# Performance work log

Hardware: AMD Instinct MI355X
Metric: run time of the kernel (lower is better)

## Reference

```python
import jax, jax.numpy as jnp
import numpy as np

B, N, M, C = 4, 4096, 300, 1152
SA_H, SA_D = 36, 32           # linear self-attention heads / head dim
CA_H = 16                     # cross-attention heads
INNER_SA = SA_H * SA_D        # 1152
INNER_FF = int(C * 2.5)       # 2880
EPS = 1e-6


def _ln(x):
    # LayerNorm without affine, eps=1e-6
    mu = x.mean(-1, keepdims=True)
    var = x.var(-1, keepdims=True)
    return (x - mu) / jnp.sqrt(var + EPS)


def setup_inputs() -> dict:
    key = jax.random.key(0)
    ks = jax.random.split(key, 24)
    p = lambda i, shape: jax.random.normal(ks[i], shape, jnp.float32) * 0.02
    return {
        "x": jax.random.normal(ks[0], (B, N, C), jnp.float32),
        "conditioning": jax.random.normal(ks[1], (B, M, C), jnp.float32),
        "t_emb": jax.random.normal(ks[2], (B, C), jnp.float32),
        # linear self-attention (qkv has no bias)
        "w_qkv": p(3, (C, 3 * INNER_SA)),
        "w_sa_out": p(4, (INNER_SA, C)),
        "b_sa_out": jnp.zeros((C,), jnp.float32),
        # norm_cross (affine LayerNorm)
        "gamma_cross": jnp.ones((C,), jnp.float32),
        "beta_cross": jnp.zeros((C,), jnp.float32),
        # cross-attention
        "w_q": p(5, (C, C)), "b_q": jnp.zeros((C,), jnp.float32),
        "w_kv": p(6, (C, 2 * C)), "b_kv": jnp.zeros((2 * C,), jnp.float32),
        "w_co": p(7, (C, C)), "b_co": jnp.zeros((C,), jnp.float32),
        # MixFFN
        "w_fc1": p(8, (C, 2 * INNER_FF)), "b_fc1": jnp.zeros((2 * INNER_FF,), jnp.float32),
        "dw_kernel": p(9, (3, 3, 1, INNER_FF)),  # depthwise conv, HWIO
        "dw_bias": jnp.zeros((INNER_FF,), jnp.float32),
        "w_fc2": p(10, (INNER_FF, C)), "b_fc2": jnp.zeros((C,), jnp.float32),
        # adaLN modulation
        "w_ada": p(11, (C, 6 * C)), "b_ada": jnp.zeros((6 * C,), jnp.float32),
        "sst": jax.random.normal(ks[12], (6, C), jnp.float32) * 0.02,
    }


def reference(x, conditioning, t_emb, w_qkv, w_sa_out, b_sa_out,
              gamma_cross, beta_cross, w_q, b_q, w_kv, b_kv, w_co, b_co,
              w_fc1, b_fc1, dw_kernel, dw_bias, w_fc2, b_fc2,
              w_ada, b_ada, sst):
    Bx, Nx, Cx = x.shape
    ada = jax.nn.silu(t_emb) @ w_ada + b_ada          # (B, 6C)
    ada = sst[None] + ada.reshape(Bx, 6, Cx)          # (B, 6, C)
    shift_sa, scale_sa, gate_sa, shift_ff, scale_ff, gate_ff = (
        ada[:, 0], ada[:, 1], ada[:, 2], ada[:, 3], ada[:, 4], ada[:, 5])

    # --- modulated linear self-attention (ReLU kernel) ---
    xn = _ln(x) * (1.0 + scale_sa[:, None]) + shift_sa[:, None]
    qkv = (xn @ w_qkv).reshape(Bx, Nx, 3, SA_H, SA_D)
    q = jax.nn.relu(qkv[:, :, 0])
    k = jax.nn.relu(qkv[:, :, 1])
    v = qkv[:, :, 2]
    kv = jnp.einsum('bnhd,bnhe->bhde', k, v)                  # (B,H,D,D)
    out = jnp.einsum('bnhd,bhde->bnhe', q, kv)                # (B,N,H,D)
    denom = jnp.einsum('bnhd,bhd->bnh', q, k.sum(1)) + 1e-6   # (B,N,H)
    out = (out / denom[..., None]).reshape(Bx, Nx, INNER_SA)
    x = x + gate_sa[:, None] * (out @ w_sa_out + b_sa_out)

    # --- cross-attention (softmax) ---
    xc = _ln(x) * gamma_cross + beta_cross
    hd = Cx // CA_H
    qc = (xc @ w_q + b_q).reshape(Bx, Nx, CA_H, hd)
    kvc = (conditioning @ w_kv + b_kv).reshape(Bx, M, 2, CA_H, hd)
    kc, vc = kvc[:, :, 0], kvc[:, :, 1]
    attn = jnp.einsum('bnhd,bmhd->bhnm', qc, kc) * (hd ** -0.5)
    attn = jax.nn.softmax(attn, axis=-1)
    oc = jnp.einsum('bhnm,bmhd->bnhd', attn, vc).reshape(Bx, Nx, Cx)
    x = x + oc @ w_co + b_co

    # --- modulated GLU-dwconv FFN ---
    xn = _ln(x) * (1.0 + scale_ff[:, None]) + shift_ff[:, None]
    gv = xn @ w_fc1 + b_fc1
    gate, val = gv[..., :INNER_FF], gv[..., INNER_FF:]
    h = jax.nn.silu(gate) * val
    hw = int(round(Nx ** 0.5))
    h = h.reshape(Bx, hw, hw, INNER_FF)                       # NHWC
    h = jax.lax.conv_general_dilated(
        h, dw_kernel, window_strides=(1, 1), padding='SAME',
        dimension_numbers=('NHWC', 'HWIO', 'NHWC'),
        feature_group_count=INNER_FF) + dw_bias
    h = h.reshape(Bx, Nx, INNER_FF)
    x = x + gate_ff[:, None] * (h @ w_fc2 + b_fc2)
    return x
```

## Files before the change

### kernel.cpp

```cpp
#include <hip/hip_runtime.h>

typedef __bf16 bf16_t;
typedef __attribute__((ext_vector_type(8))) __bf16 bf16x8;
typedef __attribute__((ext_vector_type(4))) __bf16 bf16x4;
typedef __attribute__((ext_vector_type(4))) float f32x4;

#define DEVINL __device__ __forceinline__

DEVINL void gload16(const void* g, void* l) {
  __builtin_amdgcn_global_load_lds(
      (const __attribute__((address_space(1))) void*)g,
      (__attribute__((address_space(3))) void*)l, 16, 0, 0);
}

template <int OUT>
__global__ __launch_bounds__(256) void gemm_bt(
    const bf16_t* __restrict__ A, const bf16_t* __restrict__ Bt,
    void* __restrict__ Cv, int M, int N, int K,
    long strideA, long strideB, long strideC,
    const float* __restrict__ bias, const float* __restrict__ resid,
    const float* __restrict__ gate, int GM)
{
  __shared__ __align__(16) bf16_t sA[128 * 32];
  __shared__ __align__(16) bf16_t sB[128 * 32];
  const int tid = threadIdx.x;
  const int lane = tid & 63;
  const int wave = tid >> 6;
  const bf16_t* Ab = A + (size_t)blockIdx.z * strideA;
  const bf16_t* Bb = Bt + (size_t)blockIdx.z * strideB;

  const int nbx = gridDim.x, nby = gridDim.y;
  const int nwg = nbx * nby;
  int lin = (int)blockIdx.y * nbx + (int)blockIdx.x;
  {
    const int q = nwg >> 3, r = nwg & 7;
    const int xcd = lin & 7, idx = lin >> 3;
    lin = (xcd < r ? xcd * (q + 1) : r * (q + 1) + (xcd - r) * q) + idx;
  }
  const int per_grp = GM * nbx;
  const int gid = lin / per_grp;
  const int rem = lin - gid * per_grp;
  const int gsz = min(GM, nby - gid * GM);
  const int byy = gid * GM + rem % gsz;
  const int bxx = rem / gsz;
  const long tileM = (long)byy * 128;
  const long tileN = (long)bxx * 128;
  const int wr = wave >> 1, wc = wave & 1;

  f32x4 acc[4][4] = {};

  const int srow = lane >> 2;
  const int skcol = (lane & 3) * 8;
  const bf16_t* gA0 = Ab + (tileM + wave * 16 + srow) * (long)K + skcol;
  const bf16_t* gB0 = Bb + (tileN + wave * 16 + srow) * (long)K + skcol;
  bf16_t* lA0 = sA + wave * 512;
  bf16_t* lB0 = sB + wave * 512;
  const long rs64 = 64L * K;

  const int aoff = (wr * 64 + (lane & 15)) * 32 + (lane >> 4) * 8;
  const int boff = (wc * 64 + (lane & 15)) * 32 + (lane >> 4) * 8;

  for (int kt = 0; kt < K; kt += 32) {
    __syncthreads();
    gload16(gA0 + kt, lA0);
    gload16(gA0 + kt + rs64, lA0 + 2048);
    gload16(gB0 + kt, lB0);
    gload16(gB0 + kt + rs64, lB0 + 2048);
    __syncthreads();
    bf16x8 av[4], bv[4];
#pragma unroll
    for (int m = 0; m < 4; ++m) av[m] = *(const bf16x8*)&sA[aoff + m * 512];
#pragma unroll
    for (int n = 0; n < 4; ++n) bv[n] = *(const bf16x8*)&sB[boff + n * 512];
#pragma unroll
    for (int m = 0; m < 4; ++m)
#pragma unroll
      for (int n = 0; n < 4; ++n)
        acc[m][n] = __builtin_amdgcn_mfma_f32_16x16x32_bf16(av[m], bv[n],
                                                            acc[m][n], 0, 0, 0);
  }

  const long row0 = tileM + wr * 64 + ((lane >> 4) * 4);
  const int col0 = (int)tileN + wc * 64 + (lane & 15);
#pragma unroll
  for (int m = 0; m < 4; ++m) {
#pragma unroll
    for (int n = 0; n < 4; ++n) {
      const int col = col0 + n * 16;
      const float bb = (OUT != 2 && bias) ? bias[col] : 0.0f;
#pragma unroll
      for (int j = 0; j < 4; ++j) {
        const long row = row0 + m * 16 + j;
        const float v = acc[m][n][j] + bb;
        if constexpr (OUT == 1) {
          const long idx = row * (long)N + col;
          const float g = gate ? gate[(row >> 12) * 6912 + col] : 1.0f;
          const float r = resid ? resid[idx] : 0.0f;
          ((float*)Cv)[idx] = r + g * v;
        } else if constexpr (OUT == 2) {
          if (col < 72)
            ((bf16_t*)Cv)[row * 1152 + (long)blockIdx.z * 72 + col] = (bf16_t)v;
        } else {
          const long idx = row * (long)N + col;
          (((bf16_t*)Cv) + (size_t)blockIdx.z * strideC)[idx] = (bf16_t)v;
        }
      }
    }
  }
}

__global__ __launch_bounds__(256) void transpose_cast(
    const float* __restrict__ W, bf16_t* __restrict__ WT, int K, int N)
{
  __shared__ float tile[32][33];
  const int n0 = blockIdx.x * 32, k0 = blockIdx.y * 32;
  const int tx = threadIdx.x & 31, ty = threadIdx.x >> 5;
#pragma unroll
  for (int r = ty; r < 32; r += 8) tile[r][tx] = W[(size_t)(k0 + r) * N + n0 + tx];
  __syncthreads();
#pragma unroll
  for (int r = ty; r < 32; r += 8)
    WT[(size_t)(n0 + r) * K + k0 + tx] = (bf16_t)tile[tx][r];
}

__global__ __launch_bounds__(256) void ada_kernel(
    const float* __restrict__ t_emb, const float* __restrict__ w_ada,
    const float* __restrict__ b_ada, const float* __restrict__ sst,
    float* __restrict__ ada)
{
  __shared__ float st[4][1152];
  const int t = threadIdx.x;
  const int j = blockIdx.x * 256 + t;
  for (int i = t; i < 4 * 1152; i += 256) {
    const int b = i / 1152, cc = i % 1152;
    const float v = t_emb[b * 1152 + cc];
    st[b][cc] = v / (1.0f + __expf(-v));
  }
  __syncthreads();
  const int k0 = blockIdx.y * 144;
  float a0 = 0.f, a1 = 0.f, a2 = 0.f, a3 = 0.f;
  for (int k = k0; k < k0 + 144; ++k) {
    const float w = w_ada[(size_t)k * 6912 + j];
    a0 += st[0][k] * w; a1 += st[1][k] * w;
    a2 += st[2][k] * w; a3 += st[3][k] * w;
  }
  if (blockIdx.y == 0) {
    const float base = b_ada[j] + sst[j];
    a0 += base; a1 += base; a2 += base; a3 += base;
  }
  atomicAdd(&ada[0 * 6912 + j], a0);
  atomicAdd(&ada[1 * 6912 + j], a1);
  atomicAdd(&ada[2 * 6912 + j], a2);
  atomicAdd(&ada[3 * 6912 + j], a3);
}

__global__ __launch_bounds__(256) void ln_mod(
    const float* __restrict__ X, bf16_t* __restrict__ out,
    const float* __restrict__ adaB, int shiftIdx, int scaleIdx,
    const float* __restrict__ gamma, const float* __restrict__ beta)
{
  const int row = blockIdx.x;
  const float4* xr4 = (const float4*)(X + (size_t)row * 1152);
  float s = 0.f, s2 = 0.f;
  for (int i = threadIdx.x; i < 288; i += 256) {
    const float4 v = xr4[i];
    s += v.x + v.y + v.z + v.w;
    s2 += v.x * v.x + v.y * v.y + v.z * v.z + v.w * v.w;
  }
  const int lane = threadIdx.x & 63, wave = threadIdx.x >> 6;
#pragma unroll
  for (int o = 32; o; o >>= 1) { s += __shfl_down(s, o); s2 += __shfl_down(s2, o); }
  __shared__ float rs[4], rq[4];
  if (lane == 0) { rs[wave] = s; rq[wave] = s2; }
  __syncthreads();
  if (threadIdx.x == 0) {
    rs[0] = rs[0] + rs[1] + rs[2] + rs[3];
    rq[0] = rq[0] + rq[1] + rq[2] + rq[3];
  }
  __syncthreads();
  const float mu = rs[0] * (1.0f / 1152.0f);
  const float var = rq[0] * (1.0f / 1152.0f) - mu * mu;
  const float inv = rsqrtf(var + 1e-6f);
  const int b = row >> 12;
  const float4* shiftv = (const float4*)(adaB ? adaB + b * 6912 + shiftIdx * 1152 : beta);
  const float4* scalev = (const float4*)(adaB ? adaB + b * 6912 + scaleIdx * 1152 : gamma);
  const float add1 = adaB ? 1.0f : 0.0f;
  for (int i = threadIdx.x; i < 288; i += 256) {
    const float4 v = xr4[i];
    const float4 sc = scalev[i];
    const float4 sh = shiftv[i];
    bf16x4 o;
    o[0] = (bf16_t)((v.x - mu) * inv * (add1 + sc.x) + sh.x);
    o[1] = (bf16_t)((v.y - mu) * inv * (add1 + sc.y) + sh.y);
    o[2] = (bf16_t)((v.z - mu) * inv * (add1 + sc.z) + sh.z);
    o[3] = (bf16_t)((v.w - mu) * inv * (add1 + sc.w) + sh.w);
    *(bf16x4*)&out[(size_t)row * 1152 + i * 4] = o;
  }
}

__global__ void pad_cond_k(const float* __restrict__ cond, bf16_t* __restrict__ condp)
{
  const int idx = blockIdx.x * 256 + threadIdx.x;
  const int row = idx / 1152;
  condp[idx] = (row < 1200) ? (bf16_t)cond[idx] : (bf16_t)0.0f;
}

__global__ __launch_bounds__(256) void sa_kv_k(
    const bf16_t* __restrict__ qkv, float* __restrict__ kvb, float* __restrict__ ksumb)
{
  const int bh = blockIdx.x, b = bh / 36, h = bh % 36;
  __shared__ bf16_t sk[32][32], sv[32][32];
  const int t = threadIdx.x;
  const int nn = t >> 5, c = t & 31;
  const int srow = (t & 127) >> 2;
  const int sq4 = (t & 3) * 8;
  const int isV = t >> 7;
  float a0 = 0.f, a1 = 0.f, a2 = 0.f, a3 = 0.f, ks = 0.f;
  const size_t rowbase = (size_t)b * 4096 + (size_t)blockIdx.y * 256;
  const size_t colbase = 1152 + (size_t)isV * 1152 + h * 32 + sq4;
  for (int n0 = 0; n0 < 256; n0 += 32) {
    __syncthreads();
    const bf16x8 v8 = *(const bf16x8*)&qkv[(rowbase + n0 + srow) * 3456 + colbase];
    if (isV == 0) {
      bf16x8 r8;
#pragma unroll
      for (int j = 0; j < 8; ++j) r8[j] = (bf16_t)fmaxf((float)v8[j], 0.0f);
      *(bf16x8*)&sk[srow][sq4] = r8;
    } else {
      *(bf16x8*)&sv[srow][sq4] = v8;
    }
    __syncthreads();
#pragma unroll
    for (int q = 0; q < 32; ++q) {
      const float vv = (float)sv[q][c];
      a0 += (float)sk[q][nn] * vv;
      a1 += (float)sk[q][nn + 8] * vv;
      a2 += (float)sk[q][nn + 16] * vv;
      a3 += (float)sk[q][nn + 24] * vv;
    }
    if (t < 32) {
#pragma unroll
      for (int q = 0; q < 32; ++q) ks += (float)sk[q][t];
    }
  }
  float* kvp = kvb + (size_t)bh * 1024;
  atomicAdd(&kvp[(nn + 0) * 32 + c], a0);
  atomicAdd(&kvp[(nn + 8) * 32 + c], a1);
  atomicAdd(&kvp[(nn + 16) * 32 + c], a2);
  atomicAdd(&kvp[(nn + 24) * 32 + c], a3);
  if (t < 32) atomicAdd(&ksumb[bh * 32 + t], ks);
}

__global__ __launch_bounds__(256) void sa_out_k(
    const bf16_t* __restrict__ qkv, const float* __restrict__ kvb,
    const float* __restrict__ ksumb, bf16_t* __restrict__ so)
{
  const int row0 = blockIdx.x * 8;
  const int b = row0 >> 12;
  __shared__ float q[8][1152];
  __shared__ float denom[8][36];
  const int t = threadIdx.x;
  for (int i = t; i < 1152; i += 256) {
    const int r = i / 144, c0 = (i % 144) * 8;
    const bf16x8 v8 = *(const bf16x8*)&qkv[(size_t)(row0 + r) * 3456 + c0];
#pragma unroll
    for (int j = 0; j < 8; ++j) q[r][c0 + j] = fmaxf((float)v8[j], 0.0f);
  }
  __syncthreads();
  for (int i = t; i < 288; i += 256) {
    int r = i / 36, h = i % 36;
    const float* ksp = ksumb + (b * 36 + h) * 32;
    float dsum = 1e-6f;
#pragma unroll
    for (int d = 0; d < 32; ++d) dsum += q[r][h * 32 + d] * ksp[d];
    denom[r][h] = dsum;
  }
  __syncthreads();
  for (int j = t; j < 1152; j += 256) {
    const int h = j >> 5, e = j & 31;
    const float* kvp = kvb + ((size_t)(b * 36 + h)) * 1024 + e;
    float kreg[32];
#pragma unroll
    for (int d = 0; d < 32; ++d) kreg[d] = kvp[d * 32];
#pragma unroll
    for (int r = 0; r < 8; ++r) {
      float a = 0.f;
#pragma unroll
      for (int d = 0; d < 32; ++d) a += q[r][h * 32 + d] * kreg[d];
      so[(size_t)(row0 + r) * 1152 + j] = (bf16_t)(a / denom[r][h]);
    }
  }
}

__global__ void ca_qrepack(const bf16_t* __restrict__ qc, bf16_t* __restrict__ qcp, int b)
{
  const size_t idx = (size_t)blockIdx.x * 256 + threadIdx.x;
  const int d = (int)(idx % 96);
  const size_t r = idx / 96;
  const int n = (int)(r & 4095);
  const int h = (int)(r >> 12);
  float v = 0.f;
  if (d < 72) v = (float)qc[((size_t)(b * 4096 + n)) * 1152 + h * 72 + d] * 0.11785113019775793f;
  qcp[idx] = (bf16_t)v;
}

__global__ void ca_kcrepack(const bf16_t* __restrict__ kvc, bf16_t* __restrict__ kcp, int b)
{
  const size_t idx = (size_t)blockIdx.x * 256 + threadIdx.x;
  const int d = (int)(idx % 96);
  const size_t r = idx / 96;
  const int m = (int)(r % 384);
  const int h = (int)(r / 384);
  bf16_t v = (bf16_t)0.0f;
  if (d < 72 && m < 300) v = kvc[((size_t)(b * 300 + m)) * 2304 + h * 72 + d];
  kcp[idx] = v;
}

__global__ void ca_vtrepack(const bf16_t* __restrict__ kvc, bf16_t* __restrict__ vt, int b)
{
  const size_t idx = (size_t)blockIdx.x * 256 + threadIdx.x;
  const int m = (int)(idx % 384);
  const size_t r = idx / 384;
  const int d = (int)(r & 127);
  const int h = (int)(r >> 7);
  bf16_t v = (bf16_t)0.0f;
  if (d < 72 && m < 300) v = kvc[((size_t)(b * 300 + m)) * 2304 + 1152 + h * 72 + d];
  vt[idx] = v;
}

__global__ __launch_bounds__(256) void softmax_k(bf16_t* __restrict__ s)
{
  const int row = blockIdx.x * 4 + (threadIdx.x >> 6);
  const int lane = threadIdx.x & 63;
  bf16_t* sr = s + (size_t)row * 384;
  float v[5];
  float mx = -1e30f;
#pragma unroll
  for (int i = 0; i < 5; ++i) {
    const int m = lane + 64 * i;
    v[i] = (m < 300) ? (float)sr[m] : -1e30f;
    mx = fmaxf(mx, v[i]);
  }
#pragma unroll
  for (int o = 32; o; o >>= 1) mx = fmaxf(mx, __shfl_xor(mx, o));
  float sum = 0.f;
#pragma unroll
  for (int i = 0; i < 5; ++i) { v[i] = __expf(v[i] - mx); sum += v[i]; }
#pragma unroll
  for (int o = 32; o; o >>= 1) sum += __shfl_xor(sum, o);
  const float inv = 1.0f / sum;
#pragma unroll
  for (int i = 0; i < 5; ++i) {
    const int m = lane + 64 * i;
    if (m < 320) sr[m] = (bf16_t)(v[i] * inv);
  }
}

__global__ void glu_k(const bf16_t* __restrict__ gv, bf16_t* __restrict__ h)
{
  const size_t idx = (size_t)blockIdx.x * 256 + threadIdx.x;
  const size_t row = idx / 360;
  const int c0 = (int)(idx % 360) * 8;
  const bf16x8 g8 = *(const bf16x8*)&gv[row * 5760 + c0];
  const bf16x8 v8 = *(const bf16x8*)&gv[row * 5760 + 2880 + c0];
  bf16x8 o;
#pragma unroll
  for (int j = 0; j < 8; ++j) {
    const float g = (float)g8[j];
    const float sg = g / (1.0f + __expf(-g));
    o[j] = (bf16_t)(sg * (float)v8[j]);
  }
  *(bf16x8*)&h[row * 2880 + c0] = o;
}

__global__ __launch_bounds__(256) void dwconv_k(
    const bf16_t* __restrict__ h, const float* __restrict__ wk,
    const float* __restrict__ wb, bf16_t* __restrict__ hc)
{
  const size_t idx = (size_t)blockIdx.x * 256 + threadIdx.x;
  const int c8 = (int)(idx % 360);
  size_t p = idx / 360;
  const int x = (int)(p & 63);
  const int y = (int)(p >> 6);
  const int c0 = c8 * 8;
  float acc[8];
#pragma unroll
  for (int j = 0; j < 8; ++j) acc[j] = wb[c0 + j];
  for (int ky = -1; ky <= 1; ++ky) {
    const int yy = y + ky;
    if (yy < 0 || yy > 63) continue;
    for (int kx = -1; kx <= 1; ++kx) {
      const int xx = x + kx;
      if (xx < 0 || xx > 63) continue;
      const bf16x8 v = *(const bf16x8*)&h[((size_t)(yy * 64 + xx)) * 2880 + c0];
      const float* w = wk + ((ky + 1) * 3 + (kx + 1)) * 2880 + c0;
#pragma unroll
      for (int j = 0; j < 8; ++j) acc[j] += (float)v[j] * w[j];
    }
  }
  bf16x8 o;
#pragma unroll
  for (int j = 0; j < 8; ++j) o[j] = (bf16_t)acc[j];
  *(bf16x8*)&hc[((size_t)(y * 64 + x)) * 2880 + c0] = o;
}

extern "C" void kernel_launch(void* const* d_in, const int* in_sizes, int n_in,
                              void* d_out, int out_size, void* d_ws, size_t ws_size,
                              hipStream_t stream)
{
  const float* x          = (const float*)d_in[0];
  const float* cond       = (const float*)d_in[1];
  const float* t_emb      = (const float*)d_in[2];
  const float* w_qkv      = (const float*)d_in[3];
  const float* w_sa_out   = (const float*)d_in[4];
  const float* b_sa_out   = (const float*)d_in[5];
  const float* gamma_cr   = (const float*)d_in[6];
  const float* beta_cr    = (const float*)d_in[7];
  const float* w_q        = (const float*)d_in[8];
  const float* b_q        = (const float*)d_in[9];
  const float* w_kv       = (const float*)d_in[10];
  const float* b_kv       = (const float*)d_in[11];
  const float* w_co       = (const float*)d_in[12];
  const float* b_co       = (const float*)d_in[13];
  const float* w_fc1      = (const float*)d_in[14];
  const float* b_fc1      = (const float*)d_in[15];
  const float* dw_kernel  = (const float*)d_in[16];
  const float* dw_bias    = (const float*)d_in[17];
  const float* w_fc2      = (const float*)d_in[18];
  const float* b_fc2      = (const float*)d_in[19];
  const float* w_ada      = (const float*)d_in[20];
  const float* b_ada      = (const float*)d_in[21];
  const float* sst        = (const float*)d_in[22];
  float* out = (float*)d_out;

  char* ws = (char*)d_ws;
  size_t off = 0;
  auto alloc = [&](size_t bytes) -> char* {
    off = (off + 255) & ~(size_t)255;
    char* p = ws + off;
    off += bytes;
    return p;
  };

  bf16_t* wqkvT  = (bf16_t*)alloc((size_t)3456 * 1152 * 2);
  bf16_t* wsaT   = (bf16_t*)alloc((size_t)1152 * 1152 * 2);
  bf16_t* wqT    = (bf16_t*)alloc((size_t)1152 * 1152 * 2);
  bf16_t* wkvT   = (bf16_t*)alloc((size_t)2304 * 1152 * 2);
  bf16_t* wcoT   = (bf16_t*)alloc((size_t)1152 * 1152 * 2);
  bf16_t* wfc1T  = (bf16_t*)alloc((size_t)5760 * 1152 * 2);
  bf16_t* wfc2T  = (bf16_t*)alloc((size_t)1152 * 2880 * 2);
  float*  adaB   = (float*)alloc((size_t)4 * 6912 * 4);
  bf16_t* xn     = (bf16_t*)alloc((size_t)16384 * 1152 * 2);
  bf16_t* buf37  = (bf16_t*)alloc((size_t)16384 * 1152 * 2);
  float*  kvb    = (float*)alloc((size_t)144 * 1024 * 4);
  float*  ksumb  = (float*)alloc((size_t)144 * 32 * 4);
  bf16_t* condp  = (bf16_t*)alloc((size_t)1280 * 1152 * 2);
  bf16_t* kvcB   = (bf16_t*)alloc((size_t)1280 * 2304 * 2);
  char* arena = alloc((size_t)16384 * 3456 * 2);

  if (off > ws_size) return;

  bf16_t* qkvB = (bf16_t*)arena;
  bf16_t* qcp    = (bf16_t*)arena;
  bf16_t* kcp    = (bf16_t*)(arena + 12582912);
  bf16_t* vcT    = (bf16_t*)(arena + 12582912 + 1179648);
  bf16_t* scores = (bf16_t*)(arena + 12582912 + 1179648 + 1572864);
  bf16_t* gvB = (bf16_t*)arena;
  bf16_t* hB  = (bf16_t*)(arena + (size_t)4096 * 5760 * 2);
  bf16_t* hcB = (bf16_t*)(arena + (size_t)4096 * 5760 * 2 + (size_t)4096 * 2880 * 2);

  hipMemsetAsync(adaB, 0, (size_t)4 * 6912 * 4, stream);
  hipMemsetAsync(kvb, 0, (size_t)144 * 1024 * 4, stream);
  hipMemsetAsync(ksumb, 0, (size_t)144 * 32 * 4, stream);

  transpose_cast<<<dim3(3456 / 32, 1152 / 32), 256, 0, stream>>>(w_qkv, wqkvT, 1152, 3456);
  transpose_cast<<<dim3(1152 / 32, 1152 / 32), 256, 0, stream>>>(w_sa_out, wsaT, 1152, 1152);
  transpose_cast<<<dim3(1152 / 32, 1152 / 32), 256, 0, stream>>>(w_q, wqT, 1152, 1152);
  transpose_cast<<<dim3(2304 / 32, 1152 / 32), 256, 0, stream>>>(w_kv, wkvT, 1152, 2304);
  transpose_cast<<<dim3(1152 / 32, 1152 / 32), 256, 0, stream>>>(w_co, wcoT, 1152, 1152);
  transpose_cast<<<dim3(5760 / 32, 1152 / 32), 256, 0, stream>>>(w_fc1, wfc1T, 1152, 5760);
  transpose_cast<<<dim3(1152 / 32, 2880 / 32), 256, 0, stream>>>(w_fc2, wfc2T, 2880, 1152);
  ada_kernel<<<dim3(27, 8), 256, 0, stream>>>(t_emb, w_ada, b_ada, sst, adaB);
  pad_cond_k<<<5760, 256, 0, stream>>>(cond, condp);

  ln_mod<<<16384, 256, 0, stream>>>(x, xn, adaB, 0, 1, nullptr, nullptr);
  gemm_bt<0><<<dim3(27, 128, 1), 256, 0, stream>>>(xn, wqkvT, qkvB, 16384, 3456, 1152,
                                                   0, 0, 0, nullptr, nullptr, nullptr, 8);
  sa_kv_k<<<dim3(144, 16), 256, 0, stream>>>(qkvB, kvb, ksumb);
  sa_out_k<<<2048, 256, 0, stream>>>(qkvB, kvb, ksumb, buf37);
  gemm_bt<1><<<dim3(9, 128, 1), 256, 0, stream>>>(buf37, wsaT, out, 16384, 1152, 1152,
                                                  0, 0, 0, b_sa_out, x, adaB + 2 * 1152, 8);

  ln_mod<<<16384, 256, 0, stream>>>(out, xn, nullptr, 0, 0, gamma_cr, beta_cr);
  gemm_bt<0><<<dim3(9, 128, 1), 256, 0, stream>>>(xn, wqT, buf37, 16384, 1152, 1152,
                                                  0, 0, 0, b_q, nullptr, nullptr, 8);
  gemm_bt<0><<<dim3(18, 10, 1), 256, 0, stream>>>(condp, wkvT, kvcB, 1280, 2304, 1152,
                                                  0, 0, 0, b_kv, nullptr, nullptr, 8);
  for (int b = 0; b < 4; ++b) {
    ca_qrepack<<<24576, 256, 0, stream>>>(buf37, qcp, b);
    ca_kcrepack<<<2304, 256, 0, stream>>>(kvcB, kcp, b);
    ca_vtrepack<<<3072, 256, 0, stream>>>(kvcB, vcT, b);
    gemm_bt<0><<<dim3(3, 32, 16), 256, 0, stream>>>(qcp, kcp, scores, 4096, 384, 96,
                                                    (long)4096 * 96, (long)384 * 96,
                                                    (long)4096 * 384, nullptr, nullptr, nullptr, 8);
    softmax_k<<<16384, 256, 0, stream>>>(scores);
    gemm_bt<2><<<dim3(1, 32, 16), 256, 0, stream>>>(scores, vcT,
                                                    buf37 + (size_t)b * 4096 * 1152,
                                                    4096, 128, 384,
                                                    (long)4096 * 384, (long)128 * 384,
                                                    0, nullptr, nullptr, nullptr, 8);
  }
  gemm_bt<1><<<dim3(9, 128, 1), 256, 0, stream>>>(buf37, wcoT, out, 16384, 1152, 1152,
                                                  0, 0, 0, b_co, out, nullptr, 8);

  ln_mod<<<16384, 256, 0, stream>>>(out, xn, adaB, 3, 4, nullptr, nullptr);
  for (int b = 0; b < 4; ++b) {
    gemm_bt<0><<<dim3(45, 32, 1), 256, 0, stream>>>(xn + (size_t)b * 4096 * 1152, wfc1T,
                                                    gvB, 4096, 5760, 1152,
                                                    0, 0, 0, b_fc1, nullptr, nullptr, 8);
    glu_k<<<5760, 256, 0, stream>>>(gvB, hB);
    dwconv_k<<<5760, 256, 0, stream>>>(hB, dw_kernel, dw_bias, hcB);
    gemm_bt<1><<<dim3(9, 32, 1), 256, 0, stream>>>(hcB, wfc2T, out + (size_t)b * 4096 * 1152,
                                                   4096, 1152, 2880,
                                                   0, 0, 0, b_fc2,
                                                   out + (size_t)b * 4096 * 1152,
                                                   adaB + b * 6912 + 5 * 1152, 8);
  }

  (void)in_sizes; (void)n_in; (void)out_size; (void)ws_size;
}
```

Measured before the change: 2.015 ms.

## Add double-buffered 256x256 swizzled-LDS GEMM for large projections and batch FFN fc2

Introduces a 512-thread GEMM kernel with 256x256 tiles, K-step 64 and two LDS buffers. The LDS layout is XOR-swizzled and loads are issued asynchronously with global_load_lds, with a prefetch depth of two. It replaces the 128x128 kernel for the QKV, SA-out, Q, cross-attn output, fc1 and fc2 projections, aiming for more data reuse per tile and overlap of loads with MFMA. Transposed weight buffers are padded up to multiples of 256 rows, and output columns are masked. The FFN now runs fc2 over two samples at once, writing into a larger dwconv buffer and reusing buf37 for the GLU output. The risks are the large 128KB LDS footprint, which limits occupancy, and fewer workgroups for the N=1152 GEMMs.

```diff
diff --git a/kernel.cpp b/kernel.cpp
--- a/kernel.cpp
+++ b/kernel.cpp
@@ -11,6 +11,128 @@
   __builtin_amdgcn_global_load_lds(
       (const __attribute__((address_space(1))) void*)g,
       (__attribute__((address_space(3))) void*)l, 16, 0, 0);
+}
+
+template <int OUT>
+__global__ __launch_bounds__(512) void gemm256(
+    const bf16_t* __restrict__ A, const bf16_t* __restrict__ Bt,
+    void* __restrict__ Cv, int M, int N, int K,
+    const float* __restrict__ bias, const float* __restrict__ resid,
+    const float* __restrict__ gate, int GM)
+{
+  __shared__ __align__(16) bf16_t sA[2][256 * 64];
+  __shared__ __align__(16) bf16_t sB[2][256 * 64];
+  const int tid = threadIdx.x;
+  const int lane = tid & 63;
+  const int wave = tid >> 6;
+  const int wr = wave >> 2;
+  const int wc = wave & 3;
+
+  const int nbx = gridDim.x, nby = gridDim.y;
+  const int nwg = nbx * nby;
+  int lin = (int)blockIdx.y * nbx + (int)blockIdx.x;
+  {
+    const int q = nwg >> 3, r = nwg & 7;
+    const int xcd = lin & 7, idx = lin >> 3;
+    lin = (xcd < r ? xcd * (q + 1) : r * (q + 1) + (xcd - r) * q) + idx;
+  }
+  const int per_grp = GM * nbx;
+  const int gid = lin / per_grp;
+  const int rem = lin - gid * per_grp;
+  const int gsz = min(GM, nby - gid * GM);
+  const long tileM = (long)(gid * GM + rem % gsz) * 256;
+  const long tileN = (long)(rem / gsz) * 256;
+
+  int arow[4], acol[4];
+#pragma unroll
+  for (int j = 0; j < 4; ++j) {
+    const int ch = tid + j * 512;
+    const int r = ch >> 3;
+    arow[j] = r;
+    acol[j] = ((ch & 7) ^ (r & 7)) * 8;
+  }
+
+  auto STAGE = [&](int buf, int kt) {
+#pragma unroll
+    for (int j = 0; j < 4; ++j)
+      gload16(A + (tileM + arow[j]) * (long)K + kt + acol[j],
+              (char*)(&sA[buf][0]) + (tid + j * 512) * 16);
+#pragma unroll
+    for (int j = 0; j < 4; ++j)
+      gload16(Bt + (tileN + arow[j]) * (long)K + kt + acol[j],
+              (char*)(&sB[buf][0]) + (tid + j * 512) * 16);
+  };
+
+  f32x4 acc[8][4] = {};
+  const int NT = K >> 6;
+
+  STAGE(0, 0);
+  STAGE(1, 64);
+  asm volatile("s_waitcnt vmcnt(8)" ::: "memory");
+  asm volatile("s_barrier" ::: "memory");
+
+  const int lrow = lane & 15;
+  const int lkbase = (lane >> 4) << 4;
+  const int lxor = (lane & 7) << 4;
+
+  for (int t = 0; t < NT; ++t) {
+    const char* pA = (const char*)(&sA[t & 1][0]);
+    const char* pB = (const char*)(&sB[t & 1][0]);
+#pragma unroll
+    for (int ks = 0; ks < 2; ++ks) {
+      const int koff = ((ks << 6) | lkbase) ^ lxor;
+      bf16x8 a[8], b[4];
+#pragma unroll
+      for (int n = 0; n < 4; ++n)
+        b[n] = *(const bf16x8*)(pB + (wc * 64 + n * 16 + lrow) * 128 + koff);
+#pragma unroll
+      for (int m = 0; m < 8; ++m)
+        a[m] = *(const bf16x8*)(pA + (wr * 128 + m * 16 + lrow) * 128 + koff);
+      __builtin_amdgcn_s_setprio(1);
+#pragma unroll
+      for (int m = 0; m < 8; ++m)
+#pragma unroll
+        for (int n = 0; n < 4; ++n)
+          acc[m][n] = __builtin_amdgcn_mfma_f32_16x16x32_bf16(a[m], b[n],
+                                                              acc[m][n], 0, 0, 0);
+      __builtin_amdgcn_s_setprio(0);
+    }
+    __builtin_amdgcn_sched_barrier(0);
+    asm volatile("s_barrier" ::: "memory");
+    if (t + 2 < NT) {
+      STAGE(t & 1, (t + 2) << 6);
+      asm volatile("s_waitcnt vmcnt(8)" ::: "memory");
+    } else {
+      asm volatile("s_waitcnt vmcnt(0)" ::: "memory");
+    }
+    asm volatile("s_barrier" ::: "memory");
+  }
+
+  const long row0 = tileM + wr * 128 + ((lane >> 4) * 4);
+  const int col0 = (int)tileN + wc * 64 + lrow;
+#pragma unroll
+  for (int m = 0; m < 8; ++m) {
+#pragma unroll
+    for (int n = 0; n < 4; ++n) {
+      const int col = col0 + n * 16;
+      if (col < N) {
+        const float bb = bias ? bias[col] : 0.0f;
+#pragma unroll
+        for (int j = 0; j < 4; ++j) {
+          const long row = row0 + m * 16 + j;
+          const long idx = row * (long)N + col;
+          const float v = acc[m][n][j] + bb;
+          if constexpr (OUT == 1) {
+            const float g = gate ? gate[(row >> 12) * 6912 + col] : 1.0f;
+            const float r = resid ? resid[idx] : 0.0f;
+            ((float*)Cv)[idx] = r + g * v;
+          } else {
+            ((bf16_t*)Cv)[idx] = (bf16_t)v;
+          }
+        }
+      }
+    }
+  }
 }
 
 template <int OUT>
@@ -18,8 +140,7 @@
     const bf16_t* __restrict__ A, const bf16_t* __restrict__ Bt,
     void* __restrict__ Cv, int M, int N, int K,
     long strideA, long strideB, long strideC,
-    const float* __restrict__ bias, const float* __restrict__ resid,
-    const float* __restrict__ gate, int GM)
+    const float* __restrict__ bias, int GM)
 {
   __shared__ __align__(16) bf16_t sA[128 * 32];
   __shared__ __align__(16) bf16_t sB[128 * 32];
@@ -41,10 +162,8 @@
   const int gid = lin / per_grp;
   const int rem = lin - gid * per_grp;
   const int gsz = min(GM, nby - gid * GM);
-  const int byy = gid * GM + rem % gsz;
-  const int bxx = rem / gsz;
-  const long tileM = (long)byy * 128;
-  const long tileN = (long)bxx * 128;
+  const long tileM = (long)(gid * GM + rem % gsz) * 128;
+  const long tileN = (long)(rem / gsz) * 128;
   const int wr = wave >> 1, wc = wave & 1;
 
   f32x4 acc[4][4] = {};
@@ -92,12 +211,7 @@
       for (int j = 0; j < 4; ++j) {
         const long row = row0 + m * 16 + j;
         const float v = acc[m][n][j] + bb;
-        if constexpr (OUT == 1) {
-          const long idx = row * (long)N + col;
-          const float g = gate ? gate[(row >> 12) * 6912 + col] : 1.0f;
-          const float r = resid ? resid[idx] : 0.0f;
-          ((float*)Cv)[idx] = r + g * v;
-        } else if constexpr (OUT == 2) {
+        if constexpr (OUT == 2) {
           if (col < 72)
             ((bf16_t*)Cv)[row * 1152 + (long)blockIdx.z * 72 + col] = (bf16_t)v;
         } else {
@@ -442,13 +556,13 @@
     return p;
   };
 
-  bf16_t* wqkvT  = (bf16_t*)alloc((size_t)3456 * 1152 * 2);
-  bf16_t* wsaT   = (bf16_t*)alloc((size_t)1152 * 1152 * 2);
-  bf16_t* wqT    = (bf16_t*)alloc((size_t)1152 * 1152 * 2);
+  bf16_t* wqkvT  = (bf16_t*)alloc((size_t)3584 * 1152 * 2);
+  bf16_t* wsaT   = (bf16_t*)alloc((size_t)1280 * 1152 * 2);
+  bf16_t* wqT    = (bf16_t*)alloc((size_t)1280 * 1152 * 2);
   bf16_t* wkvT   = (bf16_t*)alloc((size_t)2304 * 1152 * 2);
-  bf16_t* wcoT   = (bf16_t*)alloc((size_t)1152 * 1152 * 2);
-  bf16_t* wfc1T  = (bf16_t*)alloc((size_t)5760 * 1152 * 2);
-  bf16_t* wfc2T  = (bf16_t*)alloc((size_t)1152 * 2880 * 2);
+  bf16_t* wcoT   = (bf16_t*)alloc((size_t)1280 * 1152 * 2);
+  bf16_t* wfc1T  = (bf16_t*)alloc((size_t)5888 * 1152 * 2);
+  bf16_t* wfc2T  = (bf16_t*)alloc((size_t)1280 * 2880 * 2);
   float*  adaB   = (float*)alloc((size_t)4 * 6912 * 4);
   bf16_t* xn     = (bf16_t*)alloc((size_t)16384 * 1152 * 2);
   bf16_t* buf37  = (bf16_t*)alloc((size_t)16384 * 1152 * 2);
@@ -465,66 +579,69 @@
   bf16_t* kcp    = (bf16_t*)(arena + 12582912);
   bf16_t* vcT    = (bf16_t*)(arena + 12582912 + 1179648);
   bf16_t* scores = (bf16_t*)(arena + 12582912 + 1179648 + 1572864);
-  bf16_t* gvB = (bf16_t*)arena;
-  bf16_t* hB  = (bf16_t*)(arena + (size_t)4096 * 5760 * 2);
-  bf16_t* hcB = (bf16_t*)(arena + (size_t)4096 * 5760 * 2 + (size_t)4096 * 2880 * 2);
+  bf16_t* hc2b = (bf16_t*)arena;
+  bf16_t* gvB  = (bf16_t*)(arena + (size_t)8192 * 2880 * 2);
+  bf16_t* hB   = buf37;
 
   hipMemsetAsync(adaB, 0, (size_t)4 * 6912 * 4, stream);
   hipMemsetAsync(kvb, 0, (size_t)144 * 1024 * 4, stream);
   hipMemsetAsync(ksumb, 0, (size_t)144 * 32 * 4, stream);
 
-  transpose_cast<<<dim3(3456 / 32, 1152 / 32), 256, 0, stream>>>(w_qkv, wqkvT, 1152, 3456);
-  transpose_cast<<<dim3(1152 / 32, 1152 / 32), 256, 0, stream>>>(w_sa_out, wsaT, 1152, 1152);
-  transpose_cast<<<dim3(1152 / 32, 1152 / 32), 256, 0, stream>>>(w_q, wqT, 1152, 1152);
-  transpose_cast<<<dim3(2304 / 32, 1152 / 32), 256, 0, stream>>>(w_kv, wkvT, 1152, 2304);
-  transpose_cast<<<dim3(1152 / 32, 1152 / 32), 256, 0, stream>>>(w_co, wcoT, 1152, 1152);
-  transpose_cast<<<dim3(5760 / 32, 1152 / 32), 256, 0, stream>>>(w_fc1, wfc1T, 1152, 5760);
-  transpose_cast<<<dim3(1152 / 32, 2880 / 32), 256, 0, stream>>>(w_fc2, wfc2T, 2880, 1152);
+  transpose_cast<<<dim3(108, 36), 256, 0, stream>>>(w_qkv, wqkvT, 1152, 3456);
+  transpose_cast<<<dim3(36, 36), 256, 0, stream>>>(w_sa_out, wsaT, 1152, 1152);
+  transpose_cast<<<dim3(36, 36), 256, 0, stream>>>(w_q, wqT, 1152, 1152);
+  transpose_cast<<<dim3(72, 36), 256, 0, stream>>>(w_kv, wkvT, 1152, 2304);
+  transpose_cast<<<dim3(36, 36), 256, 0, stream>>>(w_co, wcoT, 1152, 1152);
+  transpose_cast<<<dim3(180, 36), 256, 0, stream>>>(w_fc1, wfc1T, 1152, 5760);
+  transpose_cast<<<dim3(36, 90), 256, 0, stream>>>(w_fc2, wfc2T, 2880, 1152);
   ada_kernel<<<dim3(27, 8), 256, 0, stream>>>(t_emb, w_ada, b_ada, sst, adaB);
   pad_cond_k<<<5760, 256, 0, stream>>>(cond, condp);
 
   ln_mod<<<16384, 256, 0, stream>>>(x, xn, adaB, 0, 1, nullptr, nullptr);
-  gemm_bt<0><<<dim3(27, 128, 1), 256, 0, stream>>>(xn, wqkvT, qkvB, 16384, 3456, 1152,
-                                                   0, 0, 0, nullptr, nullptr, nullptr, 8);
+  gemm256<0><<<dim3(14, 64), 512, 0, stream>>>(xn, wqkvT, qkvB, 16384, 3456, 1152,
+                                               nullptr, nullptr, nullptr, 8);
   sa_kv_k<<<dim3(144, 16), 256, 0, stream>>>(qkvB, kvb, ksumb);
   sa_out_k<<<2048, 256, 0, stream>>>(qkvB, kvb, ksumb, buf37);
-  gemm_bt<1><<<dim3(9, 128, 1), 256, 0, stream>>>(buf37, wsaT, out, 16384, 1152, 1152,
-                                                  0, 0, 0, b_sa_out, x, adaB + 2 * 1152, 8);
+  gemm256<1><<<dim3(5, 64), 512, 0, stream>>>(buf37, wsaT, out, 16384, 1152, 1152,
+                                              b_sa_out, x, adaB + 2 * 1152, 8);
 
   ln_mod<<<16384, 256, 0, stream>>>(out, xn, nullptr, 0, 0, gamma_cr, beta_cr);
-  gemm_bt<0><<<dim3(9, 128, 1), 256, 0, stream>>>(xn, wqT, buf37, 16384, 1152, 1152,
-                                                  0, 0, 0, b_q, nullptr, nullptr, 8);
+  gemm256<0><<<dim3(5, 64), 512, 0, stream>>>(xn, wqT, buf37, 16384, 1152, 1152,
+                                              b_q, nullptr, nullptr, 8);
   gemm_bt<0><<<dim3(18, 10, 1), 256, 0, stream>>>(condp, wkvT, kvcB, 1280, 2304, 1152,
-                                                  0, 0, 0, b_kv, nullptr, nullptr, 8);
+                                                  0, 0, 0, b_kv, 8);
   for (int b = 0; b < 4; ++b) {
     ca_qrepack<<<24576, 256, 0, stream>>>(buf37, qcp, b);
     ca_kcrepack<<<2304, 256, 0, stream>>>(kvcB, kcp, b);
     ca_vtrepack<<<3072, 256, 0, stream>>>(kvcB, vcT, b);
     gemm_bt<0><<<dim3(3, 32, 16), 256, 0, stream>>>(qcp, kcp, scores, 4096, 384, 96,
                                                     (long)4096 * 96, (long)384 * 96,
-                                                    (long)4096 * 384, nullptr, nullptr, nullptr, 8);
+                                                    (long)4096 * 384, nullptr, 8);
     softmax_k<<<16384, 256, 0, stream>>>(scores);
     gemm_bt<2><<<dim3(1, 32, 16), 256, 0, stream>>>(scores, vcT,
                                                     buf37 + (size_t)b * 4096 * 1152,
                                                     4096, 128, 384,
                                                     (long)4096 * 384, (long)128 * 384,
-                                                    0, nullptr, nullptr, nullptr, 8);
-  }
-  gemm_bt<1><<<dim3(9, 128, 1), 256, 0, stream>>>(buf37, wcoT, out, 16384, 1152, 1152,
-                                                  0, 0, 0, b_co, out, nullptr, 8);
+                                                    0, nullptr, 8);
+  }
+  gemm256<1><<<dim3(5, 64), 512, 0, stream>>>(buf37, wcoT, out, 16384, 1152, 1152,
+                                              b_co, out, nullptr, 8);
 
   ln_mod<<<16384, 256, 0, stream>>>(out, xn, adaB, 3, 4, nullptr, nullptr);
-  for (int b = 0; b < 4; ++b) {
-    gemm_bt<0><<<dim3(45, 32, 1), 256, 0, stream>>>(xn + (size_t)b * 4096 * 1152, wfc1T,
-                                                    gvB, 4096, 5760, 1152,
-                                                    0, 0, 0, b_fc1, nullptr, nullptr, 8);
-    glu_k<<<5760, 256, 0, stream>>>(gvB, hB);
-    dwconv_k<<<5760, 256, 0, stream>>>(hB, dw_kernel, dw_bias, hcB);
-    gemm_bt<1><<<dim3(9, 32, 1), 256, 0, stream>>>(hcB, wfc2T, out + (size_t)b * 4096 * 1152,
-                                                   4096, 1152, 2880,
-                                                   0, 0, 0, b_fc2,
-                                                   out + (size_t)b * 4096 * 1152,
-                                                   adaB + b * 6912 + 5 * 1152, 8);
+  for (int c = 0; c < 2; ++c) {
+    for (int bb = 0; bb < 2; ++bb) {
+      const int b = c * 2 + bb;
+      gemm256<0><<<dim3(23, 16), 512, 0, stream>>>(xn + (size_t)b * 4096 * 1152, wfc1T,
+                                                   gvB, 4096, 5760, 1152,
+                                                   b_fc1, nullptr, nullptr, 8);
+      glu_k<<<5760, 256, 0, stream>>>(gvB, hB);
+      dwconv_k<<<5760, 256, 0, stream>>>(hB, dw_kernel, dw_bias,
+                                         hc2b + (size_t)bb * 4096 * 2880);
+    }
+    gemm256<1><<<dim3(5, 32), 512, 0, stream>>>(hc2b, wfc2T, out + (size_t)c * 8192 * 1152,
+                                                8192, 1152, 2880, b_fc2,
+                                                out + (size_t)c * 8192 * 1152,
+                                                adaB + (size_t)c * 2 * 6912 + 5 * 1152, 8);
   }
 
   (void)in_sizes; (void)n_in; (void)out_size; (void)ws_size;
```

Result: slower. 2.065 ms (+2.5%).
